# Performance work log

Measured on AMD Instinct MI355X. Metric: run time of the kernel, lower is better.

## Reference

```python
import jax, jax.numpy as jnp
import numpy as np

D = 1280; H = 16; HD = 80; DEPTH = 4; THETA = 10000.0
GRID = [(1, 32, 32), (1, 16, 16)]  # (t, h, w) per packed image
MERGE = 2


def _pos_and_seg():
    pos, seg = [], []
    for i, (t, h, w) in enumerate(GRID):
        hp = np.arange(h)[:, None].repeat(w, 1)
        hp = hp.reshape(h // MERGE, MERGE, w // MERGE, MERGE).transpose(0, 2, 1, 3).reshape(-1)
        wp = np.arange(w)[None, :].repeat(h, 0)
        wp = wp.reshape(h // MERGE, MERGE, w // MERGE, MERGE).transpose(0, 2, 1, 3).reshape(-1)
        p = np.stack([hp, wp], -1)
        pos.append(np.tile(p, (t, 1)))
        seg.append(np.full(t * h * w, i, dtype=np.int32))
    return np.concatenate(pos, 0), np.concatenate(seg, 0)


def setup_inputs() -> dict:
    key = jax.random.key(0)
    ks = iter(jax.random.split(key, 32))
    pos_ids, seg = _pos_and_seg()
    S = pos_ids.shape[0]  # 1280
    # rotary freqs: dim = head_dim//2 = 40, 20 freqs for h-pos + 20 for w-pos
    inv_freq = 1.0 / THETA ** (np.arange(0, 40, 2, dtype=np.float32) / 40.0)  # (20,)
    max_grid = max(max(h, w) for _, h, w in GRID)
    full = np.arange(max_grid, dtype=np.float32)[:, None] * inv_freq[None, :]  # (G,20)
    rotary = full[pos_ids].reshape(S, 40)  # (S,40)
    r = lambda shape, s=0.02: jax.random.normal(next(ks), shape, jnp.float32) * s
    return {
        'pixels': jax.random.normal(next(ks), (S, 1176), jnp.float32),
        'rotary': jnp.asarray(rotary),
        'seg_ids': jnp.asarray(seg),
        'proj_w': r((D, 1176)),
        'ln1_w': jnp.ones((DEPTH, D)), 'ln1_b': jnp.zeros((DEPTH, D)),
        'qkv_w': r((DEPTH, 3 * D, D)), 'qkv_b': jnp.zeros((DEPTH, 3 * D)),
        'po_w': r((DEPTH, D, D)), 'po_b': jnp.zeros((DEPTH, D)),
        'ln2_w': jnp.ones((DEPTH, D)), 'ln2_b': jnp.zeros((DEPTH, D)),
        'fc1_w': r((DEPTH, 4 * D, D)), 'fc1_b': jnp.zeros((DEPTH, 4 * D)),
        'fc2_w': r((DEPTH, D, 4 * D)), 'fc2_b': jnp.zeros((DEPTH, D)),
        'mln_w': jnp.ones((D,)), 'mln_b': jnp.zeros((D,)),
        'm1_w': r((4 * D, 4 * D)), 'm1_b': jnp.zeros((4 * D,)),
        'm2_w': r((1536, 4 * D)), 'm2_b': jnp.zeros((1536,)),
    }


def _ln(x, w, b, eps=1e-6):
    mu = jnp.mean(x, -1, keepdims=True)
    var = jnp.var(x, -1, keepdims=True)
    return (x - mu) * jax.lax.rsqrt(var + eps) * w + b


def _rotate_half(x):
    x1, x2 = x[..., : x.shape[-1] // 2], x[..., x.shape[-1] // 2:]
    return jnp.concatenate([-x2, x1], -1)


def reference(pixels, rotary, seg_ids, proj_w, ln1_w, ln1_b, qkv_w, qkv_b, po_w, po_b,
              ln2_w, ln2_b, fc1_w, fc1_b, fc2_w, fc2_b, mln_w, mln_b, m1_w, m1_b, m2_w, m2_b):
    S = pixels.shape[0]
    # PatchEmbed: Conv3d with kernel==stride == full patch -> plain linear projection
    x = pixels @ proj_w.T  # (S, D)
    # rotary cos/sin, tiled x2 to cover full head_dim (matches repeat(1,1,2) + rotate_half)
    cos = jnp.concatenate([jnp.cos(rotary)] * 2, -1)[:, None, :]  # (S,1,80)
    sin = jnp.concatenate([jnp.sin(rotary)] * 2, -1)[:, None, :]
    rope = lambda t: t * cos + _rotate_half(t) * sin
    # block-diagonal varlen mask from cu_seqlens (tokens attend within their image only)
    mask = (seg_ids[:, None] == seg_ids[None, :])[None]  # (1,S,S)
    scale = 1.0 / jnp.sqrt(jnp.float32(HD))
    for l in range(DEPTH):
        h = _ln(x, ln1_w[l], ln1_b[l])
        qkv = (h @ qkv_w[l].T + qkv_b[l]).reshape(S, 3, H, HD)
        q, k, v = qkv[:, 0], qkv[:, 1], qkv[:, 2]  # (S,H,HD)
        q, k = rope(q), rope(k)
        scores = jnp.einsum('shd,thd->hst', q, k) * scale  # (H,S,S)
        scores = jnp.where(mask, scores, -jnp.inf)
        attn = jax.nn.softmax(scores, -1)
        o = jnp.einsum('hst,thd->shd', attn, v).reshape(S, D)
        x = x + o @ po_w[l].T + po_b[l]
        h = _ln(x, ln2_w[l], ln2_b[l])
        h = h @ fc1_w[l].T + fc1_b[l]
        h = h * jax.nn.sigmoid(1.702 * h)  # GELU(approx='fast')
        x = x + h @ fc2_w[l].T + fc2_b[l]
    # PatchMerger: LN then merge 2x2 spatial patches, MLP to hidden_size
    y = _ln(x, mln_w, mln_b).reshape(-1, D * MERGE * MERGE)  # (S/4, 5120)
    y = y @ m1_w.T + m1_b
    y = jax.nn.gelu(y, approximate=False)
    y = y @ m2_w.T + m2_b
    return y  # (S/4, 1536)
```

## Files before the change

kernel.cpp:

```cpp
#include <hip/hip_runtime.h>
#include <hip/hip_bf16.h>

typedef __bf16 bf16;
typedef __bf16 bf16x8_t __attribute__((ext_vector_type(8)));
typedef __bf16 bf16x4_t __attribute__((ext_vector_type(4)));
typedef float f32x4 __attribute__((ext_vector_type(4)));

#define S_TOK 1280
#define DMODEL 1280

__global__ __launch_bounds__(256) void cvt_pad_kernel(const float* __restrict__ src,
                                                      bf16* __restrict__ dst,
                                                      int rows, int scols, int dcols) {
  int idx = blockIdx.x * 256 + threadIdx.x;
  if (idx >= rows * dcols) return;
  int r = idx / dcols, c = idx - r * dcols;
  dst[idx] = (c < scols) ? (bf16)src[(size_t)r * scols + c] : (bf16)0.f;
}

__global__ __launch_bounds__(256) void zero_kernel(float* __restrict__ p, int n4) {
  int i = blockIdx.x * 256 + threadIdx.x;
  if (i < n4) ((float4*)p)[i] = make_float4(0.f, 0.f, 0.f, 0.f);
}

__global__ __launch_bounds__(256) void gelu_cvt_kernel(const float* __restrict__ in,
                                                       bf16* __restrict__ out, int n4) {
  int i = blockIdx.x * 256 + threadIdx.x;
  if (i >= n4) return;
  float4 v = ((const float4*)in)[i];
  bf16x4_t o;
  o[0] = (bf16)(0.5f * v.x * (1.f + erff(v.x * 0.70710678f)));
  o[1] = (bf16)(0.5f * v.y * (1.f + erff(v.y * 0.70710678f)));
  o[2] = (bf16)(0.5f * v.z * (1.f + erff(v.z * 0.70710678f)));
  o[3] = (bf16)(0.5f * v.w * (1.f + erff(v.w * 0.70710678f)));
  *(bf16x4_t*)&out[(size_t)i * 4] = o;
}

__global__ __launch_bounds__(256) void ln_kernel(const float* __restrict__ x,
                                                 const float* __restrict__ w,
                                                 const float* __restrict__ b,
                                                 bf16* __restrict__ out) {
  __shared__ float ls[4], ls2[4];
  int row = blockIdx.x;
  const float* xr = x + (size_t)row * DMODEL;
  float v[5];
  float s = 0.f, s2 = 0.f;
#pragma unroll
  for (int i = 0; i < 5; i++) {
    v[i] = xr[i * 256 + threadIdx.x];
    s += v[i];
    s2 += v[i] * v[i];
  }
#pragma unroll
  for (int off = 32; off; off >>= 1) {
    s += __shfl_down(s, off);
    s2 += __shfl_down(s2, off);
  }
  int wv = threadIdx.x >> 6;
  if ((threadIdx.x & 63) == 0) { ls[wv] = s; ls2[wv] = s2; }
  __syncthreads();
  float ts = ls[0] + ls[1] + ls[2] + ls[3];
  float ts2 = ls2[0] + ls2[1] + ls2[2] + ls2[3];
  float mu = ts * (1.f / DMODEL);
  float var = ts2 * (1.f / DMODEL) - mu * mu;
  float rstd = rsqrtf(var + 1e-6f);
#pragma unroll
  for (int i = 0; i < 5; i++) {
    int c = i * 256 + threadIdx.x;
    out[(size_t)row * DMODEL + c] = (bf16)((v[i] - mu) * rstd * w[c] + b[c]);
  }
}

__global__ __launch_bounds__(256) void rope_kernel(bf16* __restrict__ qkv,
                                                   const float* __restrict__ rotary) {
  int idx = blockIdx.x * 256 + threadIdx.x;
  if (idx >= S_TOK * 16 * 40) return;
  int d = idx % 40;
  int h = (idx / 40) & 15;
  int s = idx / (40 * 16);
  float ang = rotary[s * 40 + d];
  float c = cosf(ang), sn = sinf(ang);
#pragma unroll
  for (int qk = 0; qk < 2; ++qk) {
    bf16* base = qkv + (size_t)s * 3840 + qk * 1280 + h * 80;
    float t1 = (float)base[d], t2 = (float)base[d + 40];
    base[d] = (bf16)(t1 * c - t2 * sn);
    base[d + 40] = (bf16)(t2 * c + t1 * sn);
  }
}

template <int EPI, typename TB>
__global__ __launch_bounds__(256, 2) void gemm_bt(const bf16* __restrict__ A,
                                                  const TB* __restrict__ B,
                                                  const float* __restrict__ bias,
                                                  float* __restrict__ Cf,
                                                  bf16* __restrict__ Cb,
                                                  int M, int N, int K) {
  constexpr int BKP = 40;
  __shared__ bf16 As[128 * BKP];
  __shared__ bf16 Bs[128 * BKP];
  const int tid = threadIdx.x;
  const int bm = blockIdx.x, bn = blockIdx.y;
  const int wave = tid >> 6, lane = tid & 63;
  const int wm = (wave & 1) << 6, wn = (wave >> 1) << 6;
  const int lm = lane & 15, quad = lane >> 4;
  f32x4 acc[4][4] = {};
  const int lrow = tid >> 2;
  const int lcol = (tid & 3) * 8;
  const int arow0 = bm * 128 + lrow;
  const int brow0 = bn * 128 + lrow;
  const int Kc = K / gridDim.z;
  const int kbeg = blockIdx.z * Kc;
  const int kend = kbeg + Kc;

  for (int k0 = kbeg; k0 < kend; k0 += 32) {
#pragma unroll
    for (int p = 0; p < 2; p++) {
      int ar = arow0 + p * 64;
      if (ar > M - 1) ar = M - 1;
      *(bf16x8_t*)&As[(p * 64 + lrow) * BKP + lcol] =
          *(const bf16x8_t*)&A[(size_t)ar * K + k0 + lcol];
      if constexpr (sizeof(TB) == 2) {
        *(bf16x8_t*)&Bs[(p * 64 + lrow) * BKP + lcol] =
            *(const bf16x8_t*)&B[(size_t)(brow0 + p * 64) * K + k0 + lcol];
      } else {
        const float* bp = (const float*)&B[(size_t)(brow0 + p * 64) * K + k0 + lcol];
        float4 f0 = *(const float4*)bp;
        float4 f1 = *(const float4*)(bp + 4);
        bf16x8_t bv;
        bv[0] = (bf16)f0.x; bv[1] = (bf16)f0.y; bv[2] = (bf16)f0.z; bv[3] = (bf16)f0.w;
        bv[4] = (bf16)f1.x; bv[5] = (bf16)f1.y; bv[6] = (bf16)f1.z; bv[7] = (bf16)f1.w;
        *(bf16x8_t*)&Bs[(p * 64 + lrow) * BKP + lcol] = bv;
      }
    }
    __syncthreads();
    bf16x8_t af[4], bfv[4];
#pragma unroll
    for (int i = 0; i < 4; i++) {
      af[i] = *(const bf16x8_t*)&As[(wm + i * 16 + lm) * BKP + quad * 8];
      bfv[i] = *(const bf16x8_t*)&Bs[(wn + i * 16 + lm) * BKP + quad * 8];
    }
#pragma unroll
    for (int i = 0; i < 4; i++)
#pragma unroll
      for (int j = 0; j < 4; j++)
        acc[i][j] = __builtin_amdgcn_mfma_f32_16x16x32_bf16(af[i], bfv[j], acc[i][j], 0, 0, 0);
    __syncthreads();
  }

#pragma unroll
  for (int j = 0; j < 4; j++) {
    int n = bn * 128 + wn + j * 16 + lm;
    float bv = (bias != nullptr && blockIdx.z == 0) ? bias[n] : 0.f;
#pragma unroll
    for (int i = 0; i < 4; i++) {
      int mbase = bm * 128 + wm + i * 16 + quad * 4;
#pragma unroll
      for (int r = 0; r < 4; r++) {
        int m = mbase + r;
        if (m >= M) continue;
        float v = acc[i][j][r] + bv;
        size_t idx = (size_t)m * N + n;
        if constexpr (EPI == 1) {
          Cb[idx] = (bf16)v;
        } else if constexpr (EPI == 2) {
          atomicAdd(&Cf[idx], v);
        } else {
          float sv = v / (1.f + __expf(-1.702f * v));
          Cb[idx] = (bf16)sv;
        }
      }
    }
  }
}

__global__ __launch_bounds__(256) void attn_kernel(const bf16* __restrict__ qkv,
                                                   bf16* __restrict__ o) {
  constexpr int QSTR = 104;
  constexpr int VSTR = 72;
  __shared__ bf16 Qs[64 * QSTR];
  __shared__ bf16 Ks[64 * QSTR];
  __shared__ bf16 Vt[80 * VSTR];
  __shared__ bf16 Ps[4 * 16 * 64];
  const int h = blockIdx.y;
  const int qt = blockIdx.x;
  const int q0 = qt * 64;
  const int kbeg = (q0 < 1024) ? 0 : 1024;
  const int kend = (q0 < 1024) ? 1024 : 1280;
  const int tid = threadIdx.x, wave = tid >> 6, lane = tid & 63;
  const int lm = lane & 15, quad = lane >> 4;

  for (int slot = tid; slot < 64 * 13; slot += 256) {
    int r = slot / 13, c = slot - r * 13;
    bf16x8_t val = {};
    if (c < 10) val = *(const bf16x8_t*)&qkv[(size_t)(q0 + r) * 3840 + h * 80 + c * 8];
    *(bf16x8_t*)&Qs[r * QSTR + c * 8] = val;
  }

  f32x4 oacc[5] = {};
  float mrow[4], lsum[4];
#pragma unroll
  for (int r = 0; r < 4; r++) { mrow[r] = -1e30f; lsum[r] = 0.f; }
  const float scale = 0.11180339887498949f;

  for (int t0 = kbeg; t0 < kend; t0 += 64) {
    __syncthreads();
    for (int slot = tid; slot < 64 * 13; slot += 256) {
      int r = slot / 13, c = slot - r * 13;
      bf16x8_t val = {};
      if (c < 10) val = *(const bf16x8_t*)&qkv[(size_t)(t0 + r) * 3840 + 1280 + h * 80 + c * 8];
      *(bf16x8_t*)&Ks[r * QSTR + c * 8] = val;
    }
    for (int slot = tid; slot < 64 * 10; slot += 256) {
      int r = slot / 10, c = slot - r * 10;
      bf16x8_t val = *(const bf16x8_t*)&qkv[(size_t)(t0 + r) * 3840 + 2560 + h * 80 + c * 8];
#pragma unroll
      for (int j = 0; j < 8; j++) Vt[(c * 8 + j) * VSTR + r] = val[j];
    }
    __syncthreads();

    f32x4 sc[4] = {};
#pragma unroll
    for (int ks = 0; ks < 3; ks++) {
      bf16x8_t aq = *(const bf16x8_t*)&Qs[(wave * 16 + lm) * QSTR + ks * 32 + quad * 8];
#pragma unroll
      for (int j = 0; j < 4; j++) {
        bf16x8_t bk = *(const bf16x8_t*)&Ks[(j * 16 + lm) * QSTR + ks * 32 + quad * 8];
        sc[j] = __builtin_amdgcn_mfma_f32_16x16x32_bf16(aq, bk, sc[j], 0, 0, 0);
      }
    }
#pragma unroll
    for (int j = 0; j < 4; j++) sc[j] *= scale;

    float alpha[4];
#pragma unroll
    for (int r = 0; r < 4; r++) {
      float mx = fmaxf(fmaxf(sc[0][r], sc[1][r]), fmaxf(sc[2][r], sc[3][r]));
#pragma unroll
      for (int off = 8; off; off >>= 1) mx = fmaxf(mx, __shfl_xor(mx, off));
      float mn = fmaxf(mrow[r], mx);
      alpha[r] = __expf(mrow[r] - mn);
      mrow[r] = mn;
      float rsum = 0.f;
#pragma unroll
      for (int j = 0; j < 4; j++) {
        float p = __expf(sc[j][r] - mn);
        sc[j][r] = p;
        rsum += p;
      }
#pragma unroll
      for (int off = 8; off; off >>= 1) rsum += __shfl_xor(rsum, off);
      lsum[r] = lsum[r] * alpha[r] + rsum;
    }

#pragma unroll
    for (int j = 0; j < 4; j++)
#pragma unroll
      for (int r = 0; r < 4; r++)
        Ps[wave * 1024 + (quad * 4 + r) * 64 + j * 16 + lm] = (bf16)sc[j][r];
#pragma unroll
    for (int jf = 0; jf < 5; jf++)
#pragma unroll
      for (int r = 0; r < 4; r++) oacc[jf][r] *= alpha[r];
    __syncthreads();

#pragma unroll
    for (int ks = 0; ks < 2; ks++) {
      bf16x8_t ap = *(const bf16x8_t*)&Ps[wave * 1024 + lm * 64 + ks * 32 + quad * 8];
#pragma unroll
      for (int jf = 0; jf < 5; jf++) {
        bf16x8_t bv = *(const bf16x8_t*)&Vt[(jf * 16 + lm) * VSTR + ks * 32 + quad * 8];
        oacc[jf] = __builtin_amdgcn_mfma_f32_16x16x32_bf16(ap, bv, oacc[jf], 0, 0, 0);
      }
    }
  }

#pragma unroll
  for (int jf = 0; jf < 5; jf++)
#pragma unroll
    for (int r = 0; r < 4; r++) {
      int q = q0 + wave * 16 + quad * 4 + r;
      int d = jf * 16 + lm;
      o[(size_t)q * DMODEL + h * 80 + d] = (bf16)(oacc[jf][r] / lsum[r]);
    }
}

extern "C" void kernel_launch(void* const* d_in, const int* in_sizes, int n_in,
                              void* d_out, int out_size, void* d_ws, size_t ws_size,
                              hipStream_t stream) {
  const float* pixels = (const float*)d_in[0];
  const float* rotary = (const float*)d_in[1];
  const float* proj_w = (const float*)d_in[3];
  const float* ln1_w = (const float*)d_in[4];
  const float* ln1_b = (const float*)d_in[5];
  const float* qkv_w = (const float*)d_in[6];
  const float* qkv_b = (const float*)d_in[7];
  const float* po_w = (const float*)d_in[8];
  const float* po_b = (const float*)d_in[9];
  const float* ln2_w = (const float*)d_in[10];
  const float* ln2_b = (const float*)d_in[11];
  const float* fc1_w = (const float*)d_in[12];
  const float* fc1_b = (const float*)d_in[13];
  const float* fc2_w = (const float*)d_in[14];
  const float* fc2_b = (const float*)d_in[15];
  const float* mln_w = (const float*)d_in[16];
  const float* mln_b = (const float*)d_in[17];
  const float* m1_w = (const float*)d_in[18];
  const float* m1_b = (const float*)d_in[19];
  const float* m2_w = (const float*)d_in[20];
  const float* m2_b = (const float*)d_in[21];

  char* ws = (char*)d_ws;
  float* x = (float*)ws;   ws += (size_t)1280 * 1280 * 4;
  bf16* hb = (bf16*)ws;    ws += (size_t)1280 * 1280 * 2;
  bf16* shared = (bf16*)ws;
  bf16* qkvb = shared;
  bf16* h4b = shared;
  bf16* ob = hb;
  bf16* padA = shared;
  bf16* padW = shared + (size_t)1280 * 1280;

  dim3 blk(256);
  cvt_pad_kernel<<<(1280 * 1280) / 256, blk, 0, stream>>>(pixels, padA, 1280, 1176, 1280);
  cvt_pad_kernel<<<(1280 * 1280) / 256, blk, 0, stream>>>(proj_w, padW, 1280, 1176, 1280);
  zero_kernel<<<1600, blk, 0, stream>>>(x, 1280 * 1280 / 4);
  gemm_bt<2, bf16><<<dim3(10, 10, 4), blk, 0, stream>>>(padA, padW, nullptr, x, nullptr,
                                                        1280, 1280, 1280);

  for (int l = 0; l < 4; l++) {
    ln_kernel<<<1280, blk, 0, stream>>>(x, ln1_w + l * 1280, ln1_b + l * 1280, hb);
    gemm_bt<1, float><<<dim3(10, 30, 1), blk, 0, stream>>>(hb, qkv_w + (size_t)l * 3840 * 1280,
                                                           qkv_b + l * 3840, nullptr, qkvb,
                                                           1280, 3840, 1280);
    rope_kernel<<<(1280 * 16 * 40) / 256, blk, 0, stream>>>(qkvb, rotary);
    attn_kernel<<<dim3(20, 16), blk, 0, stream>>>(qkvb, ob);
    gemm_bt<2, float><<<dim3(10, 10, 4), blk, 0, stream>>>(ob, po_w + (size_t)l * 1280 * 1280,
                                                           po_b + l * 1280, x, nullptr,
                                                           1280, 1280, 1280);
    ln_kernel<<<1280, blk, 0, stream>>>(x, ln2_w + l * 1280, ln2_b + l * 1280, hb);
    gemm_bt<3, float><<<dim3(10, 40, 1), blk, 0, stream>>>(hb, fc1_w + (size_t)l * 5120 * 1280,
                                                           fc1_b + l * 5120, nullptr, h4b,
                                                           1280, 5120, 1280);
    gemm_bt<2, float><<<dim3(10, 10, 8), blk, 0, stream>>>(h4b, fc2_w + (size_t)l * 1280 * 5120,
                                                           fc2_b + l * 1280, x, nullptr,
                                                           1280, 1280, 5120);
  }

  ln_kernel<<<1280, blk, 0, stream>>>(x, mln_w, mln_b, hb);
  zero_kernel<<<1600, blk, 0, stream>>>(x, 320 * 5120 / 4);
  gemm_bt<2, float><<<dim3(3, 40, 8), blk, 0, stream>>>(hb, m1_w, m1_b, x, nullptr,
                                                        320, 5120, 5120);
  gelu_cvt_kernel<<<1600, blk, 0, stream>>>(x, h4b, 320 * 5120 / 4);
  zero_kernel<<<480, blk, 0, stream>>>((float*)d_out, 320 * 1536 / 4);
  gemm_bt<2, float><<<dim3(3, 12, 16), blk, 0, stream>>>(h4b, m2_w, m2_b, (float*)d_out, nullptr,
                                                         320, 1536, 5120);
}
```

Before: 1.828 ms.

## Split-K QKV and FC1 GEMMs with fp32 scratch plus XCD-aware block remap

Remaps the flat workgroup index so that consecutive tiles land on the same XCD, aiming for better L2 reuse across the chiplets. When the workspace is large enough, the QKV and FC1 GEMMs are split along K into two slices that accumulate atomically into an fp32 scratch buffer. Separate epilogue kernels then add the bias and apply RoPE or swish, converting to bf16. The split doubles block count to raise parallelism, but it adds a zeroing pass, atomic traffic and an extra fp32 read and write of the output.

```diff
diff --git a/kernel.cpp b/kernel.cpp
--- a/kernel.cpp
+++ b/kernel.cpp
@@ -36,6 +36,48 @@
   *(bf16x4_t*)&out[(size_t)i * 4] = o;
 }
 
+__global__ __launch_bounds__(256) void swish_cvt_kernel(const float* __restrict__ in,
+                                                        const float* __restrict__ bias,
+                                                        bf16* __restrict__ out,
+                                                        int n4, int cols4) {
+  int i = blockIdx.x * 256 + threadIdx.x;
+  if (i >= n4) return;
+  float4 v = ((const float4*)in)[i];
+  int c = (i % cols4) * 4;
+  const float4 bb = *(const float4*)&bias[c];
+  float a0 = v.x + bb.x, a1 = v.y + bb.y, a2 = v.z + bb.z, a3 = v.w + bb.w;
+  bf16x4_t o;
+  o[0] = (bf16)(a0 / (1.f + __expf(-1.702f * a0)));
+  o[1] = (bf16)(a1 / (1.f + __expf(-1.702f * a1)));
+  o[2] = (bf16)(a2 / (1.f + __expf(-1.702f * a2)));
+  o[3] = (bf16)(a3 / (1.f + __expf(-1.702f * a3)));
+  *(bf16x4_t*)&out[(size_t)i * 4] = o;
+}
+
+__global__ __launch_bounds__(256) void qkv_epi_kernel(const float* __restrict__ qkvf,
+                                                      const float* __restrict__ bias,
+                                                      const float* __restrict__ rotary,
+                                                      bf16* __restrict__ qkvb) {
+  int idx = blockIdx.x * 256 + threadIdx.x;
+  if (idx >= S_TOK * 16 * 40) return;
+  int d = idx % 40;
+  int h = (idx / 40) & 15;
+  int s = idx / 640;
+  float ang = rotary[s * 40 + d];
+  float c = cosf(ang), sn = sinf(ang);
+  size_t base = (size_t)s * 3840 + h * 80;
+  float q1 = qkvf[base + d] + bias[h * 80 + d];
+  float q2 = qkvf[base + d + 40] + bias[h * 80 + d + 40];
+  qkvb[base + d] = (bf16)(q1 * c - q2 * sn);
+  qkvb[base + d + 40] = (bf16)(q2 * c + q1 * sn);
+  float k1 = qkvf[base + 1280 + d] + bias[1280 + h * 80 + d];
+  float k2 = qkvf[base + 1280 + d + 40] + bias[1280 + h * 80 + d + 40];
+  qkvb[base + 1280 + d] = (bf16)(k1 * c - k2 * sn);
+  qkvb[base + 1280 + d + 40] = (bf16)(k2 * c + k1 * sn);
+  qkvb[base + 2560 + d] = (bf16)(qkvf[base + 2560 + d] + bias[2560 + h * 80 + d]);
+  qkvb[base + 2560 + d + 40] = (bf16)(qkvf[base + 2560 + d + 40] + bias[2560 + h * 80 + d + 40]);
+}
+
 __global__ __launch_bounds__(256) void ln_kernel(const float* __restrict__ x,
                                                  const float* __restrict__ w,
                                                  const float* __restrict__ b,
@@ -100,7 +142,16 @@
   __shared__ bf16 As[128 * BKP];
   __shared__ bf16 Bs[128 * BKP];
   const int tid = threadIdx.x;
-  const int bm = blockIdx.x, bn = blockIdx.y;
+
+  unsigned nwg = gridDim.x * gridDim.y * gridDim.z;
+  unsigned flat = blockIdx.x + gridDim.x * (blockIdx.y + gridDim.y * blockIdx.z);
+  unsigned qq = nwg >> 3, rr = nwg & 7u;
+  unsigned xcd = flat & 7u, off = flat >> 3;
+  unsigned wg = (xcd < rr ? xcd * (qq + 1) : rr * (qq + 1) + (xcd - rr) * qq) + off;
+  const int bm = wg % gridDim.x;
+  const int bn = (wg / gridDim.x) % gridDim.y;
+  const int bz = wg / (gridDim.x * gridDim.y);
+
   const int wave = tid >> 6, lane = tid & 63;
   const int wm = (wave & 1) << 6, wn = (wave >> 1) << 6;
   const int lm = lane & 15, quad = lane >> 4;
@@ -110,7 +161,7 @@
   const int arow0 = bm * 128 + lrow;
   const int brow0 = bn * 128 + lrow;
   const int Kc = K / gridDim.z;
-  const int kbeg = blockIdx.z * Kc;
+  const int kbeg = bz * Kc;
   const int kend = kbeg + Kc;
 
   for (int k0 = kbeg; k0 < kend; k0 += 32) {
@@ -151,7 +202,7 @@
 #pragma unroll
   for (int j = 0; j < 4; j++) {
     int n = bn * 128 + wn + j * 16 + lm;
-    float bv = (bias != nullptr && blockIdx.z == 0) ? bias[n] : 0.f;
+    float bv = (bias != nullptr && bz == 0) ? bias[n] : 0.f;
 #pragma unroll
     for (int i = 0; i < 4; i++) {
       int mbase = bm * 128 + wm + i * 16 + quad * 4;
@@ -313,12 +364,14 @@
   char* ws = (char*)d_ws;
   float* x = (float*)ws;   ws += (size_t)1280 * 1280 * 4;
   bf16* hb = (bf16*)ws;    ws += (size_t)1280 * 1280 * 2;
-  bf16* shared = (bf16*)ws;
+  bf16* shared = (bf16*)ws; ws += (size_t)1280 * 5120 * 2;
   bf16* qkvb = shared;
   bf16* h4b = shared;
   bf16* ob = hb;
   bf16* padA = shared;
   bf16* padW = shared + (size_t)1280 * 1280;
+  float* fscr = (float*)ws;
+  const bool big_ws = ws_size >= (size_t)49152000;
 
   dim3 blk(256);
   cvt_pad_kernel<<<(1280 * 1280) / 256, blk, 0, stream>>>(pixels, padA, 1280, 1176, 1280);
@@ -329,18 +382,35 @@
 
   for (int l = 0; l < 4; l++) {
     ln_kernel<<<1280, blk, 0, stream>>>(x, ln1_w + l * 1280, ln1_b + l * 1280, hb);
-    gemm_bt<1, float><<<dim3(10, 30, 1), blk, 0, stream>>>(hb, qkv_w + (size_t)l * 3840 * 1280,
-                                                           qkv_b + l * 3840, nullptr, qkvb,
-                                                           1280, 3840, 1280);
-    rope_kernel<<<(1280 * 16 * 40) / 256, blk, 0, stream>>>(qkvb, rotary);
+    if (big_ws) {
+      zero_kernel<<<4800, blk, 0, stream>>>(fscr, 1280 * 3840 / 4);
+      gemm_bt<2, float><<<dim3(10, 30, 2), blk, 0, stream>>>(hb, qkv_w + (size_t)l * 3840 * 1280,
+                                                             nullptr, fscr, nullptr,
+                                                             1280, 3840, 1280);
+      qkv_epi_kernel<<<3200, blk, 0, stream>>>(fscr, qkv_b + l * 3840, rotary, qkvb);
+    } else {
+      gemm_bt<1, float><<<dim3(10, 30, 1), blk, 0, stream>>>(hb, qkv_w + (size_t)l * 3840 * 1280,
+                                                             qkv_b + l * 3840, nullptr, qkvb,
+                                                             1280, 3840, 1280);
+      rope_kernel<<<(1280 * 16 * 40) / 256, blk, 0, stream>>>(qkvb, rotary);
+    }
     attn_kernel<<<dim3(20, 16), blk, 0, stream>>>(qkvb, ob);
     gemm_bt<2, float><<<dim3(10, 10, 4), blk, 0, stream>>>(ob, po_w + (size_t)l * 1280 * 1280,
                                                            po_b + l * 1280, x, nullptr,
                                                            1280, 1280, 1280);
     ln_kernel<<<1280, blk, 0, stream>>>(x, ln2_w + l * 1280, ln2_b + l * 1280, hb);
-    gemm_bt<3, float><<<dim3(10, 40, 1), blk, 0, stream>>>(hb, fc1_w + (size_t)l * 5120 * 1280,
-                                                           fc1_b + l * 5120, nullptr, h4b,
-                                                           1280, 5120, 1280);
+    if (big_ws) {
+      zero_kernel<<<6400, blk, 0, stream>>>(fscr, 1280 * 5120 / 4);
+      gemm_bt<2, float><<<dim3(10, 40, 2), blk, 0, stream>>>(hb, fc1_w + (size_t)l * 5120 * 1280,
+                                                             nullptr, fscr, nullptr,
+                                                             1280, 5120, 1280);
+      swish_cvt_kernel<<<6400, blk, 0, stream>>>(fscr, fc1_b + l * 5120, h4b,
+                                                 1280 * 5120 / 4, 5120 / 4);
+    } else {
+      gemm_bt<3, float><<<dim3(10, 40, 1), blk, 0, stream>>>(hb, fc1_w + (size_t)l * 5120 * 1280,
+                                                             fc1_b + l * 5120, nullptr, h4b,
+                                                             1280, 5120, 1280);
+    }
     gemm_bt<2, float><<<dim3(10, 10, 8), blk, 0, stream>>>(h4b, fc2_w + (size_t)l * 1280 * 5120,
                                                            fc2_b + l * 1280, x, nullptr,
                                                            1280, 1280, 5120);
```

Result: slower. 1.891 ms (+3.4%).

## Split-KV attention with merge kernel, pre-transposed V, and XCD-aware GEMM tile remap

Applied to the files above, without the earlier changes.

Attention for the 1024-token image is split into four 256-key chunks, each run by its own block and written as fp32 partial outputs plus row max and sum. A new merge kernel rescales and combines the partials. This raises attention grid parallelism from 320 blocks to 1088. The QKV GEMM epilogue also writes V transposed into a separate buffer, so attention can load V^T with vector loads instead of scattering it into shared memory. The P buffer stride gets padding to cut bank conflicts, and GEMM block indices are remapped so neighbouring tiles land on the same XCD. The cost is extra workspace, an extra launch, and fp32 partial traffic.

```diff
diff --git a/kernel.cpp b/kernel.cpp
--- a/kernel.cpp
+++ b/kernel.cpp
@@ -95,12 +95,22 @@
                                                   const float* __restrict__ bias,
                                                   float* __restrict__ Cf,
                                                   bf16* __restrict__ Cb,
+                                                  bf16* __restrict__ Vtb,
                                                   int M, int N, int K) {
   constexpr int BKP = 40;
   __shared__ bf16 As[128 * BKP];
   __shared__ bf16 Bs[128 * BKP];
   const int tid = threadIdx.x;
-  const int bm = blockIdx.x, bn = blockIdx.y;
+
+  unsigned nwg = gridDim.x * gridDim.y * gridDim.z;
+  unsigned flat = blockIdx.x + gridDim.x * (blockIdx.y + gridDim.y * blockIdx.z);
+  unsigned qq = nwg >> 3, rr = nwg & 7u;
+  unsigned xcd = flat & 7u, off = flat >> 3;
+  unsigned wg = (xcd < rr ? xcd * (qq + 1) : rr * (qq + 1) + (xcd - rr) * qq) + off;
+  const int bm = wg % gridDim.x;
+  const int bn = (wg / gridDim.x) % gridDim.y;
+  const int bz = wg / (gridDim.x * gridDim.y);
+
   const int wave = tid >> 6, lane = tid & 63;
   const int wm = (wave & 1) << 6, wn = (wave >> 1) << 6;
   const int lm = lane & 15, quad = lane >> 4;
@@ -110,7 +120,7 @@
   const int arow0 = bm * 128 + lrow;
   const int brow0 = bn * 128 + lrow;
   const int Kc = K / gridDim.z;
-  const int kbeg = blockIdx.z * Kc;
+  const int kbeg = bz * Kc;
   const int kend = kbeg + Kc;
 
   for (int k0 = kbeg; k0 < kend; k0 += 32) {
@@ -151,10 +161,17 @@
 #pragma unroll
   for (int j = 0; j < 4; j++) {
     int n = bn * 128 + wn + j * 16 + lm;
-    float bv = (bias != nullptr && blockIdx.z == 0) ? bias[n] : 0.f;
+    float bv = (bias != nullptr && bz == 0) ? bias[n] : 0.f;
 #pragma unroll
     for (int i = 0; i < 4; i++) {
       int mbase = bm * 128 + wm + i * 16 + quad * 4;
+      if (EPI == 1 && Vtb != nullptr && n >= 2560) {
+        bf16x4_t pv;
+#pragma unroll
+        for (int r = 0; r < 4; r++) pv[r] = (bf16)(acc[i][j][r] + bv);
+        *(bf16x4_t*)&Vtb[(size_t)(n - 2560) * 1280 + mbase] = pv;
+        continue;
+      }
 #pragma unroll
       for (int r = 0; r < 4; r++) {
         int m = mbase + r;
@@ -175,18 +192,28 @@
 }
 
 __global__ __launch_bounds__(256) void attn_kernel(const bf16* __restrict__ qkv,
-                                                   bf16* __restrict__ o) {
+                                                   const bf16* __restrict__ vtb,
+                                                   bf16* __restrict__ o,
+                                                   float* __restrict__ opart,
+                                                   float* __restrict__ ml) {
   constexpr int QSTR = 104;
   constexpr int VSTR = 72;
+  constexpr int PSTR = 72;
   __shared__ bf16 Qs[64 * QSTR];
   __shared__ bf16 Ks[64 * QSTR];
   __shared__ bf16 Vt[80 * VSTR];
-  __shared__ bf16 Ps[4 * 16 * 64];
-  const int h = blockIdx.y;
-  const int qt = blockIdx.x;
+  __shared__ bf16 Ps[4 * 16 * PSTR];
+  const int bid = blockIdx.x;
+  int qt, h, kbeg;
+  bool partial;
+  if (bid < 1024) {
+    int sp = bid >> 8, rem = bid & 255;
+    h = rem >> 4; qt = rem & 15; kbeg = sp * 256; partial = true;
+  } else {
+    int j = bid - 1024;
+    h = j >> 2; qt = 16 + (j & 3); kbeg = 1024; partial = false;
+  }
   const int q0 = qt * 64;
-  const int kbeg = (q0 < 1024) ? 0 : 1024;
-  const int kend = (q0 < 1024) ? 1024 : 1280;
   const int tid = threadIdx.x, wave = tid >> 6, lane = tid & 63;
   const int lm = lane & 15, quad = lane >> 4;
 
@@ -203,7 +230,8 @@
   for (int r = 0; r < 4; r++) { mrow[r] = -1e30f; lsum[r] = 0.f; }
   const float scale = 0.11180339887498949f;
 
-  for (int t0 = kbeg; t0 < kend; t0 += 64) {
+  for (int tt = 0; tt < 4; ++tt) {
+    const int t0 = kbeg + tt * 64;
     __syncthreads();
     for (int slot = tid; slot < 64 * 13; slot += 256) {
       int r = slot / 13, c = slot - r * 13;
@@ -211,11 +239,10 @@
       if (c < 10) val = *(const bf16x8_t*)&qkv[(size_t)(t0 + r) * 3840 + 1280 + h * 80 + c * 8];
       *(bf16x8_t*)&Ks[r * QSTR + c * 8] = val;
     }
-    for (int slot = tid; slot < 64 * 10; slot += 256) {
-      int r = slot / 10, c = slot - r * 10;
-      bf16x8_t val = *(const bf16x8_t*)&qkv[(size_t)(t0 + r) * 3840 + 2560 + h * 80 + c * 8];
-#pragma unroll
-      for (int j = 0; j < 8; j++) Vt[(c * 8 + j) * VSTR + r] = val[j];
+    for (int slot = tid; slot < 80 * 8; slot += 256) {
+      int d = slot >> 3, c = slot & 7;
+      *(bf16x8_t*)&Vt[d * VSTR + c * 8] =
+          *(const bf16x8_t*)&vtb[(size_t)(h * 80 + d) * 1280 + t0 + c * 8];
     }
     __syncthreads();
 
@@ -257,7 +284,7 @@
     for (int j = 0; j < 4; j++)
 #pragma unroll
       for (int r = 0; r < 4; r++)
-        Ps[wave * 1024 + (quad * 4 + r) * 64 + j * 16 + lm] = (bf16)sc[j][r];
+        Ps[wave * 16 * PSTR + (quad * 4 + r) * PSTR + j * 16 + lm] = (bf16)sc[j][r];
 #pragma unroll
     for (int jf = 0; jf < 5; jf++)
 #pragma unroll
@@ -266,7 +293,7 @@
 
 #pragma unroll
     for (int ks = 0; ks < 2; ks++) {
-      bf16x8_t ap = *(const bf16x8_t*)&Ps[wave * 1024 + lm * 64 + ks * 32 + quad * 8];
+      bf16x8_t ap = *(const bf16x8_t*)&Ps[wave * 16 * PSTR + lm * PSTR + ks * 32 + quad * 8];
 #pragma unroll
       for (int jf = 0; jf < 5; jf++) {
         bf16x8_t bv = *(const bf16x8_t*)&Vt[(jf * 16 + lm) * VSTR + ks * 32 + quad * 8];
@@ -275,14 +302,68 @@
     }
   }
 
-#pragma unroll
-  for (int jf = 0; jf < 5; jf++)
-#pragma unroll
-    for (int r = 0; r < 4; r++) {
-      int q = q0 + wave * 16 + quad * 4 + r;
-      int d = jf * 16 + lm;
-      o[(size_t)q * DMODEL + h * 80 + d] = (bf16)(oacc[jf][r] / lsum[r]);
-    }
+  if (partial) {
+#pragma unroll
+    for (int jf = 0; jf < 5; jf++)
+#pragma unroll
+      for (int r = 0; r < 4; r++) {
+        int row = wave * 16 + quad * 4 + r;
+        opart[(size_t)bid * 5120 + row * 80 + jf * 16 + lm] = oacc[jf][r];
+      }
+    if (lm == 0) {
+#pragma unroll
+      for (int r = 0; r < 4; r++) {
+        int row = wave * 16 + quad * 4 + r;
+        ml[bid * 128 + row * 2] = mrow[r];
+        ml[bid * 128 + row * 2 + 1] = lsum[r];
+      }
+    }
+  } else {
+#pragma unroll
+    for (int jf = 0; jf < 5; jf++)
+#pragma unroll
+      for (int r = 0; r < 4; r++) {
+        int q = q0 + wave * 16 + quad * 4 + r;
+        int d = jf * 16 + lm;
+        o[(size_t)q * DMODEL + h * 80 + d] = (bf16)(oacc[jf][r] / lsum[r]);
+      }
+  }
+}
+
+__global__ __launch_bounds__(256) void attn_merge_kernel(const float* __restrict__ opart,
+                                                         const float* __restrict__ ml,
+                                                         bf16* __restrict__ o) {
+  int i = blockIdx.x * 256 + threadIdx.x;
+  if (i >= 327680) return;
+  int d4 = i % 20;
+  int q = (i / 20) & 63;
+  int h = (i / 1280) & 15;
+  int qt = i / 20480;
+  int jb = h * 16 + qt;
+  float mm[4], llv[4];
+#pragma unroll
+  for (int s = 0; s < 4; s++) {
+    mm[s] = ml[(s * 256 + jb) * 128 + q * 2];
+    llv[s] = ml[(s * 256 + jb) * 128 + q * 2 + 1];
+  }
+  float mstar = fmaxf(fmaxf(mm[0], mm[1]), fmaxf(mm[2], mm[3]));
+  float w[4], L = 0.f;
+#pragma unroll
+  for (int s = 0; s < 4; s++) {
+    w[s] = __expf(mm[s] - mstar);
+    L += llv[s] * w[s];
+  }
+  float4 acc = make_float4(0.f, 0.f, 0.f, 0.f);
+#pragma unroll
+  for (int s = 0; s < 4; s++) {
+    const float4 v = *(const float4*)&opart[(size_t)(s * 256 + jb) * 5120 + q * 80 + d4 * 4];
+    acc.x += w[s] * v.x; acc.y += w[s] * v.y; acc.z += w[s] * v.z; acc.w += w[s] * v.w;
+  }
+  float inv = 1.f / L;
+  bf16x4_t ov;
+  ov[0] = (bf16)(acc.x * inv); ov[1] = (bf16)(acc.y * inv);
+  ov[2] = (bf16)(acc.z * inv); ov[3] = (bf16)(acc.w * inv);
+  *(bf16x4_t*)&o[(size_t)(qt * 64 + q) * DMODEL + h * 80 + d4 * 4] = ov;
 }
 
 extern "C" void kernel_launch(void* const* d_in, const int* in_sizes, int n_in,
@@ -313,45 +394,49 @@
   char* ws = (char*)d_ws;
   float* x = (float*)ws;   ws += (size_t)1280 * 1280 * 4;
   bf16* hb = (bf16*)ws;    ws += (size_t)1280 * 1280 * 2;
-  bf16* shared = (bf16*)ws;
+  bf16* shared = (bf16*)ws; ws += (size_t)1280 * 5120 * 2;
   bf16* qkvb = shared;
+  bf16* vtb = shared + (size_t)1280 * 3840;
   bf16* h4b = shared;
   bf16* ob = hb;
   bf16* padA = shared;
   bf16* padW = shared + (size_t)1280 * 1280;
+  float* opart = (float*)ws;  ws += (size_t)1024 * 5120 * 4;
+  float* mlbuf = (float*)ws;  ws += (size_t)1024 * 128 * 4;
 
   dim3 blk(256);
   cvt_pad_kernel<<<(1280 * 1280) / 256, blk, 0, stream>>>(pixels, padA, 1280, 1176, 1280);
   cvt_pad_kernel<<<(1280 * 1280) / 256, blk, 0, stream>>>(proj_w, padW, 1280, 1176, 1280);
   zero_kernel<<<1600, blk, 0, stream>>>(x, 1280 * 1280 / 4);
   gemm_bt<2, bf16><<<dim3(10, 10, 4), blk, 0, stream>>>(padA, padW, nullptr, x, nullptr,
-                                                        1280, 1280, 1280);
+                                                        nullptr, 1280, 1280, 1280);
 
   for (int l = 0; l < 4; l++) {
     ln_kernel<<<1280, blk, 0, stream>>>(x, ln1_w + l * 1280, ln1_b + l * 1280, hb);
     gemm_bt<1, float><<<dim3(10, 30, 1), blk, 0, stream>>>(hb, qkv_w + (size_t)l * 3840 * 1280,
                                                            qkv_b + l * 3840, nullptr, qkvb,
-                                                           1280, 3840, 1280);
+                                                           vtb, 1280, 3840, 1280);
     rope_kernel<<<(1280 * 16 * 40) / 256, blk, 0, stream>>>(qkvb, rotary);
-    attn_kernel<<<dim3(20, 16), blk, 0, stream>>>(qkvb, ob);
+    attn_kernel<<<1088, blk, 0, stream>>>(qkvb, vtb, ob, opart, mlbuf);
+    attn_merge_kernel<<<1280, blk, 0, stream>>>(opart, mlbuf, ob);
     gemm_bt<2, float><<<dim3(10, 10, 4), blk, 0, stream>>>(ob, po_w + (size_t)l * 1280 * 1280,
                                                            po_b + l * 1280, x, nullptr,
-                                                           1280, 1280, 1280);
+                                                           nullptr, 1280, 1280, 1280);
     ln_kernel<<<1280, blk, 0, stream>>>(x, ln2_w + l * 1280, ln2_b + l * 1280, hb);
     gemm_bt<3, float><<<dim3(10, 40, 1), blk, 0, stream>>>(hb, fc1_w + (size_t)l * 5120 * 1280,
                                                            fc1_b + l * 5120, nullptr, h4b,
-                                                           1280, 5120, 1280);
+                                                           nullptr, 1280, 5120, 1280);
     gemm_bt<2, float><<<dim3(10, 10, 8), blk, 0, stream>>>(h4b, fc2_w + (size_t)l * 1280 * 5120,
                                                            fc2_b + l * 1280, x, nullptr,
-                                                           1280, 1280, 5120);
+                                                           nullptr, 1280, 1280, 5120);
   }
 
   ln_kernel<<<1280, blk, 0, stream>>>(x, mln_w, mln_b, hb);
   zero_kernel<<<1600, blk, 0, stream>>>(x, 320 * 5120 / 4);
   gemm_bt<2, float><<<dim3(3, 40, 8), blk, 0, stream>>>(hb, m1_w, m1_b, x, nullptr,
-                                                        320, 5120, 5120);
+                                                        nullptr, 320, 5120, 5120);
   gelu_cvt_kernel<<<1600, blk, 0, stream>>>(x, h4b, 320 * 5120 / 4);
   zero_kernel<<<480, blk, 0, stream>>>((float*)d_out, 320 * 1536 / 4);
   gemm_bt<2, float><<<dim3(3, 12, 16), blk, 0, stream>>>(h4b, m2_w, m2_b, (float*)d_out, nullptr,
-                                                         320, 1536, 5120);
-}
+                                                         nullptr, 320, 1536, 5120);
+}
```

After: 1.617 ms. 11.6% less time.
